# Optimization experiments

Measured on AMD Instinct MI355X. Metric: run time of the kernel, lower is better.

The kernel has to match this reference:

```python
import jax, jax.numpy as jnp
import numpy as np
from jax import lax

EPS = 1e-5

def conv2d(x, w, stride=1, pad=0):
    return lax.conv_general_dilated(x, w, (stride, stride), [(pad, pad), (pad, pad)],
                                    dimension_numbers=('NCHW', 'OIHW', 'NCHW'))

def bn_silu(x, p):
    # p: [4, C] = (gamma, beta, running_mean, running_var), eval-mode BN + SiLU
    g, b, m, v = p[0], p[1], p[2], p[3]
    scale = (g / jnp.sqrt(v + EPS))[None, :, None, None]
    y = (x - m[None, :, None, None]) * scale + b[None, :, None, None]
    return y * jax.nn.sigmoid(y)

def pixel_shuffle(x, r):
    N, C, H, W = x.shape
    C2 = C // (r * r)
    return x.reshape(N, C2, r, r, H, W).transpose(0, 1, 4, 2, 5, 3).reshape(N, C2, H * r, W * r)

def carafe_upsample(x, w_down, b_down, w_enc, b_enc, w_out, b_out, k=3, up=2):
    N, C, H, W = x.shape
    kt = conv2d(x, w_down) + b_down[None, :, None, None]            # [N, C//4, H, W]
    kt = conv2d(kt, w_enc, pad=k // 2) + b_enc[None, :, None, None]  # [N, up^2*k^2, H, W]
    kt = pixel_shuffle(kt, up)                                      # [N, k^2, H*up, W*up]
    kt = jax.nn.softmax(kt, axis=1)
    k2 = k * k
    # gather the up x up sub-blocks back per low-res position: [N, k2, H, W, up^2]
    kt = kt.reshape(N, k2, H, up, W, up).transpose(0, 1, 2, 4, 3, 5).reshape(N, k2, H, W, up * up)
    kt = kt.transpose(0, 2, 3, 1, 4)                                # [N, H, W, k2, up^2]
    # overlapping k x k input patches, zero-padded: [N, C*k2, H, W] with (C, kh, kw) channel order
    patches = lax.conv_general_dilated_patches(x, (k, k), (1, 1), [(k // 2, k // 2)] * 2)
    patches = patches.reshape(N, C, k2, H, W).transpose(0, 3, 4, 1, 2)  # [N, H, W, C, k2]
    out = jnp.einsum('nhwck,nhwkq->nhwcq', patches, kt)             # [N, H, W, C, up^2]
    out = out.reshape(N, H, W, C * up * up).transpose(0, 3, 1, 2)   # [N, C*up^2, H, W]
    out = pixel_shuffle(out, up)                                    # [N, C, H*up, W*up]
    return conv2d(out, w_out) + b_out[None, :, None, None]

def asff2_forward(input1, input2, w_down, b_down, w_enc, b_enc, w_up_out, b_up_out,
                  w_l1, bn_l1, w_l2, bn_l2, w_wl, b_wl, w_conv, bn_conv):
    # level == 0: upsample input2 to input1's resolution
    input2u = carafe_upsample(input2, w_down, b_down, w_enc, b_enc, w_up_out, b_up_out)
    v1 = bn_silu(conv2d(input1, w_l1), bn_l1)        # [N, 8, H, W]
    v2 = bn_silu(conv2d(input2u, w_l2), bn_l2)       # [N, 8, H, W]
    v = jnp.concatenate([v1, v2], axis=1)            # [N, 16, H, W]
    lw = conv2d(v, w_wl) + b_wl[None, :, None, None]  # [N, 2, H, W]
    lw = jax.nn.softmax(lw, axis=1)
    fused = input1 * lw[:, 0:1] + input2u * lw[:, 1:2]
    return bn_silu(conv2d(fused, w_conv, pad=1), bn_conv)


def _bn_params(key, c):
    ks = jax.random.split(key, 4)
    return jnp.stack([jax.random.uniform(ks[0], (c,)) + 0.5,
                      0.1 * jax.random.normal(ks[1], (c,)),
                      0.1 * jax.random.normal(ks[2], (c,)),
                      jax.random.uniform(ks[3], (c,)) + 0.5])


def setup_inputs() -> dict:
    key = jax.random.key(0)
    ks = jax.random.split(key, 20)
    N, C1, C2, H, W = 8, 256, 512, 64, 64
    s = 0.05  # small weight scale for numerical stability
    return {
        'input1': jax.random.normal(ks[0], (N, C1, H, W), jnp.float32),
        'input2': jax.random.normal(ks[1], (N, C2, H // 2, W // 2), jnp.float32),
        'w_down': s * jax.random.normal(ks[2], (C2 // 4, C2, 1, 1), jnp.float32),
        'b_down': s * jax.random.normal(ks[3], (C2 // 4,), jnp.float32),
        'w_enc': s * jax.random.normal(ks[4], (36, C2 // 4, 3, 3), jnp.float32),
        'b_enc': s * jax.random.normal(ks[5], (36,), jnp.float32),
        'w_up_out': s * jax.random.normal(ks[6], (C1, C2, 1, 1), jnp.float32),
        'b_up_out': s * jax.random.normal(ks[7], (C1,), jnp.float32),
        'w_l1': s * jax.random.normal(ks[8], (8, C1, 1, 1), jnp.float32),
        'bn_l1': _bn_params(ks[9], 8),
        'w_l2': s * jax.random.normal(ks[10], (8, C1, 1, 1), jnp.float32),
        'bn_l2': _bn_params(ks[11], 8),
        'w_wl': s * jax.random.normal(ks[12], (2, 16, 1, 1), jnp.float32),
        'b_wl': s * jax.random.normal(ks[13], (2,), jnp.float32),
        'w_conv': s * jax.random.normal(ks[14], (C1, C1, 3, 3), jnp.float32),
        'bn_conv': _bn_params(ks[15], C1),
    }


def reference(input1, input2, w_down, b_down, w_enc, b_enc, w_up_out, b_up_out,
              w_l1, bn_l1, w_l2, bn_l2, w_wl, b_wl, w_conv, bn_conv):
    return asff2_forward(input1, input2, w_down, b_down, w_enc, b_enc, w_up_out, b_up_out,
                         w_l1, bn_l1, w_l2, bn_l2, w_wl, b_wl, w_conv, bn_conv)
```

## Files before the change

### kernel.cpp

```cpp
#include <hip/hip_runtime.h>
#include <math.h>


#define EPS 1e-5f
typedef unsigned short u16;
typedef __attribute__((ext_vector_type(8))) __bf16 bf16x8;
typedef __attribute__((ext_vector_type(4))) float f32x4;

#define VMCNT(N) asm volatile("s_waitcnt vmcnt(" #N ")" ::: "memory")

__device__ inline u16 f2bf(float x) {
    union { float f; unsigned u; } v; v.f = x;
    unsigned r = v.u + 0x7FFF + ((v.u >> 16) & 1);
    return (u16)(r >> 16);
}
__device__ inline float bf2f(u16 x) {
    union { unsigned u; float f; } v; v.u = (unsigned)x << 16; return v.f;
}

#define STAGE_A(dstp, t, kx)                                                         \
    {                                                                                \
        const u16* Abase = A + ((long)(t) * 256 + rowBase) * KCC + (kx) * 32;        \
        _Pragma("unroll")                                                            \
        for (int ii = 0; ii < 2; ++ii) {                                             \
            int f = ii * 256 + tid;                                                  \
            int r = f >> 2, uu = f & 3;                                              \
            __builtin_amdgcn_global_load_lds(                                        \
                (const __attribute__((address_space(1))) void*)                      \
                    (Abase + (long)r * KCC + ((uu ^ ((r >> 1) & 3)) << 3)),          \
                (__attribute__((address_space(3))) void*)((dstp) + f * 8),           \
                16, 0, 0);                                                           \
        }                                                                            \
    }

#define STAGE_B(dstp, kx)                                                            \
    {                                                                                \
        const u16* Bbase = Bn + (long)g0 * KCC + (kx) * 32;                          \
        for (int f = tid; f < BUNITS; f += 256) {                                    \
            int r = f >> 2, uu = f & 3;                                              \
            __builtin_amdgcn_global_load_lds(                                        \
                (const __attribute__((address_space(1))) void*)                      \
                    (Bbase + (long)r * KCC + ((uu ^ ((r >> 1) & 3)) << 3)),          \
                (__attribute__((address_space(3))) void*)((dstp) + f * 8),           \
                16, 0, 0);                                                           \
        }                                                                            \
    }

__global__ __launch_bounds__(256, 2) void lowres_gemm_kernel(
    const u16* __restrict__ Aup,
    const u16* __restrict__ Adn,
    const u16* __restrict__ B,
    const float* __restrict__ bias,
    u16* __restrict__ Z,
    u16* __restrict__ ktT)
{
    constexpr int KCC = 512;
    constexpr int BUNITS = 512;
    __shared__ __align__(16) u16 lsA[3][128 * 32];
    __shared__ __align__(16) u16 lsB[3][128 * 32];
    const int n = blockIdx.z;
    const u16* Bn = B + (long)n * 1024 * 512;
    const int tid = threadIdx.x;
    const int lane = tid & 63;
    const int wid = tid >> 6;
    const int mw = wid >> 1, nw = wid & 1;
    const int lr = lane & 15, lk = lane >> 4;
    const int ybr = blockIdx.y;
    const u16* A = (ybr < 2) ? Aup : Adn;
    const int rowBase = (ybr < 2) ? ybr * 128 : 0;
    const int colBase = blockIdx.x * 128;
    const int g0 = colBase;

    STAGE_A(lsA[0], 0, 0); STAGE_B(lsB[0], 0);
    STAGE_A(lsA[1], 0, 1); STAGE_B(lsB[1], 1);

    const int aswz = (lk ^ ((lr >> 1) & 3)) << 3;
    int aoff[4];
#pragma unroll
    for (int mf = 0; mf < 4; ++mf)
        aoff[mf] = (mw * 64 + mf * 16 + lr) * 32 + aswz;

    f32x4 acc[4][4] = {};
    for (int kx = 0; kx < 16; ++kx) {
        if (kx == 15) { VMCNT(0); } else { VMCNT(4); }
        __builtin_amdgcn_s_barrier();
        asm volatile("" ::: "memory");
        if (kx + 2 < 16) {
            STAGE_A(lsA[(kx + 2) % 3], 0, kx + 2);
            STAGE_B(lsB[(kx + 2) % 3], kx + 2);
        }
        const u16* la = lsA[kx % 3];
        const u16* lb = lsB[kx % 3];
        bf16x8 af[4], bfr[4];
#pragma unroll
        for (int mf = 0; mf < 4; ++mf)
            af[mf] = *(const bf16x8*)(la + aoff[mf]);
        const int rb = nw * 64 + lr;
        const int bswz = (lk ^ ((rb >> 1) & 3)) << 3;
#pragma unroll
        for (int nf = 0; nf < 4; ++nf)
            bfr[nf] = *(const bf16x8*)(lb + (rb + nf * 16) * 32 + bswz);
#pragma unroll
        for (int mf = 0; mf < 4; ++mf)
#pragma unroll
            for (int nf = 0; nf < 4; ++nf)
                acc[mf][nf] = __builtin_amdgcn_mfma_f32_16x16x32_bf16(
                    af[mf], bfr[nf], acc[mf][nf], 0, 0, 0);
    }

    if (ybr < 2) {
        u16* Zn = Z + (long)n * 1024 * 256;
#pragma unroll
        for (int mf = 0; mf < 4; ++mf) {
            const int co0 = rowBase + mw * 64 + mf * 16 + lk * 4;
#pragma unroll
            for (int nf = 0; nf < 4; ++nf) {
                const int col = colBase + nw * 64 + nf * 16 + lr;
                unsigned lo = (unsigned)f2bf(acc[mf][nf][0]) |
                              ((unsigned)f2bf(acc[mf][nf][1]) << 16);
                unsigned hi = (unsigned)f2bf(acc[mf][nf][2]) |
                              ((unsigned)f2bf(acc[mf][nf][3]) << 16);
                *(uint2*)(Zn + (long)col * 256 + co0) = make_uint2(lo, hi);
            }
        }
    } else {
        u16* Kn = ktT + (long)n * 1156 * 128;
#pragma unroll
        for (int mf = 0; mf < 4; ++mf) {
            const int co0 = mw * 64 + mf * 16 + lk * 4;
            float b0 = bias[co0], b1 = bias[co0 + 1], b2 = bias[co0 + 2], b3 = bias[co0 + 3];
#pragma unroll
            for (int nf = 0; nf < 4; ++nf) {
                const int col = colBase + nw * 64 + nf * 16 + lr;
                const int pr = ((col >> 5) + 1) * 34 + (col & 31) + 1;
                unsigned lo = (unsigned)f2bf(acc[mf][nf][0] + b0) |
                              ((unsigned)f2bf(acc[mf][nf][1] + b1) << 16);
                unsigned hi = (unsigned)f2bf(acc[mf][nf][2] + b2) |
                              ((unsigned)f2bf(acc[mf][nf][3] + b3) << 16);
                *(uint2*)(Kn + (long)pr * 128 + co0) = make_uint2(lo, hi);
            }
        }
    }
}

__global__ __launch_bounds__(64) void encsm_zw_kernel(
    const u16* __restrict__ A, const u16* __restrict__ B,
    const float* __restrict__ bias,
    const u16* __restrict__ zbfT, const float* __restrict__ wl2T,
    float* __restrict__ mask, float* __restrict__ zwT)
{
    const int bid = blockIdx.x;
    const int lane = threadIdx.x;
    if (bid < 512) {
        const int n = bid >> 6;
        const int lr = lane & 15, lk = lane >> 4;
        const int p = (bid & 63) * 16 + lr;
        const int pr = ((p >> 5) + 1) * 34 + (p & 31) + 1;
        const u16* Bn = B + (long)n * 1156 * 128;
        const int bOff = pr * 128 + lk * 8;
        f32x4 acc[3] = {};
        for (int t = 0; t < 9; ++t) {
            const u16* At = A + t * 8192;
            const int btap = ((t / 3 - 1) * 34 + (t % 3 - 1)) * 128;
#pragma unroll
            for (int k0 = 0; k0 < 128; k0 += 32) {
                bf16x8 bf = *(const bf16x8*)(Bn + bOff + btap + k0);
#pragma unroll
                for (int mf = 0; mf < 3; ++mf) {
                    bf16x8 af = *(const bf16x8*)(At + (mf * 16 + lr) * 128 + lk * 8 + k0);
                    acc[mf] = __builtin_amdgcn_mfma_f32_16x16x32_bf16(af, bf, acc[mf], 0, 0, 0);
                }
            }
        }
        float* mp = mask + ((long)n * 1024 + p) * 36;
#pragma unroll
        for (int q = 0; q < 4; ++q) {
            float v0 = acc[0][q] + bias[lk * 4 + q];
            float v1 = acc[1][q] + bias[16 + lk * 4 + q];
            float v2 = (lk == 0) ? (acc[2][q] + bias[32 + q]) : -1e30f;
            float m = fmaxf(fmaxf(v0, v1), v2);
            m = fmaxf(m, __shfl_xor(m, 16, 64));
            m = fmaxf(m, __shfl_xor(m, 32, 64));
            float e0 = expf(v0 - m);
            float e1 = expf(v1 - m);
            float e2 = (lk == 0) ? expf(v2 - m) : 0.f;
            float s = e0 + e1 + e2;
            s += __shfl_xor(s, 16, 64);
            s += __shfl_xor(s, 32, 64);
            float inv = 1.f / s;
            mp[lk * 4 + q] = e0 * inv;
            mp[16 + lk * 4 + q] = e1 * inv;
            if (lk == 0) mp[32 + q] = e2 * inv;
        }
    } else {
        const int Q = bid - 512;
        const int ci0 = lane * 4;
        uint2 v = *(const uint2*)(zbfT + (long)Q * 256 + ci0);
        float c[4] = { bf2f((u16)(v.x & 0xffff)), bf2f((u16)(v.x >> 16)),
                       bf2f((u16)(v.y & 0xffff)), bf2f((u16)(v.y >> 16)) };
        float s[8] = {};
#pragma unroll
        for (int t = 0; t < 4; ++t) {
            const float* wr = wl2T + (ci0 + t) * 8;
            float4 wa = *(const float4*)wr;
            float4 wb = *(const float4*)(wr + 4);
            s[0] += wa.x * c[t]; s[1] += wa.y * c[t]; s[2] += wa.z * c[t]; s[3] += wa.w * c[t];
            s[4] += wb.x * c[t]; s[5] += wb.y * c[t]; s[6] += wb.z * c[t]; s[7] += wb.w * c[t];
        }
#pragma unroll
        for (int off = 1; off < 64; off <<= 1)
#pragma unroll
            for (int j = 0; j < 8; ++j)
                s[j] += __shfl_xor(s[j], off, 64);
        if (lane == 0) {
            float* o = zwT + (long)Q * 8;
            *(float4*)o = make_float4(s[0], s[1], s[2], s[3]);
            *(float4*)(o + 4) = make_float4(s[4], s[5], s[6], s[7]);
        }
    }
}

__global__ __launch_bounds__(256) void carafe_fuse_blend_kernel(
    const float* __restrict__ i1g, const u16* __restrict__ zbfT,
    const float* __restrict__ zwT, const float* __restrict__ maskb,
    const float* __restrict__ bnp,
    const float* __restrict__ w_l1, const float* __restrict__ bn_l1,
    const float* __restrict__ bn_l2, const float* __restrict__ w_wl,
    const float* __restrict__ b_wl, u16* __restrict__ dst)
{
    __shared__ float lw0s[32];
    __shared__ __align__(16) unsigned char uscr[32 * 264 * 2];
    float* red = (float*)uscr;
    u16* lds2 = (u16*)uscr;
    const int n = blockIdx.y;
    const int h = blockIdx.x >> 1;
    const int w0 = (blockIdx.x & 1) << 5;
    const int hq = h >> 1;
    const int tid = threadIdx.x;

    const int w = tid & 31;
    const int chunk = tid >> 5;
    const float* i1 = i1g + (long)n * 256 * 4096 + (h << 6) + w0 + w;
    float i1v[32];
    {
        float s1[8] = {};
#pragma unroll
        for (int i = 0; i < 32; ++i) {
            const int ci = chunk * 32 + i;
            float x1 = i1[(long)ci * 4096];
            i1v[i] = x1;
#pragma unroll
            for (int j = 0; j < 8; ++j) s1[j] += w_l1[j * 256 + ci] * x1;
        }
#pragma unroll
        for (int j = 0; j < 8; ++j) red[(chunk * 32 + w) * 8 + j] = s1[j];
    }
    __syncthreads();
    {
        int px = tid >> 3, j = tid & 7;
        float s = 0.f;
#pragma unroll
        for (int o = 0; o < 8; ++o) s += red[(o * 32 + px) * 8 + j];
        red[px * 8 + j] = s;
    }
    __syncthreads();
    if (tid < 32) {
        const int wp = w0 + tid;
        const int wq = wp >> 1;
        const int q = ((h & 1) << 1) | (wp & 1);
        const float* mrow = maskb + ((long)n * 1024 + hq * 32 + wq) * 36;
        float v[16];
#pragma unroll
        for (int j = 0; j < 8; ++j) v[j] = red[tid * 8 + j];
#pragma unroll
        for (int j = 0; j < 8; ++j) v[8 + j] = bnp[512 + j];
#pragma unroll
        for (int k = 0; k < 9; ++k) {
            int dh = k / 3 - 1, dw = k - (k / 3) * 3 - 1;
            int gr = hq + dh, gc = wq + dw;
            bool ok = (gr >= 0 && gr < 32 && gc >= 0 && gc < 32);
            float mk = ok ? mrow[k * 4 + q] : 0.f;
            const float* zp = zwT + ((long)n * 1024 +
                                     (ok ? gr * 32 + gc : hq * 32 + wq)) * 8;
            float4 za = *(const float4*)zp;
            float4 zb = *(const float4*)(zp + 4);
            v[8]  += mk * za.x; v[9]  += mk * za.y; v[10] += mk * za.z; v[11] += mk * za.w;
            v[12] += mk * zb.x; v[13] += mk * zb.y; v[14] += mk * zb.z; v[15] += mk * zb.w;
        }
        float z0 = b_wl[0], z1 = b_wl[1];
#pragma unroll
        for (int j = 0; j < 8; ++j) {
            float g = bn_l1[j], b = bn_l1[8 + j], m = bn_l1[16 + j], va = bn_l1[24 + j];
            float y = (v[j] - m) * (g * rsqrtf(va + EPS)) + b;
            float sv = y / (1.f + expf(-y));
            z0 += w_wl[j] * sv;
            z1 += w_wl[16 + j] * sv;
            g = bn_l2[j]; b = bn_l2[8 + j]; m = bn_l2[16 + j]; va = bn_l2[24 + j];
            y = (v[8 + j] - m) * (g * rsqrtf(va + EPS)) + b;
            sv = y / (1.f + expf(-y));
            z0 += w_wl[8 + j] * sv;
            z1 += w_wl[24 + j] * sv;
        }
        lw0s[tid] = 1.f / (1.f + expf(z1 - z0));
    }
    __syncthreads();
    {
        const float lw = lw0s[w], lw1 = 1.f - lw;
        const int wp = w0 + w;
        const int wq = wp >> 1;
        const int q = ((h & 1) << 1) | (wp & 1);
        const float* mrow = maskb + ((long)n * 1024 + hq * 32 + wq) * 36;
        float m9[9];
        const u16* zp[9];
#pragma unroll
        for (int k = 0; k < 9; ++k) {
            int dh = k / 3 - 1, dw = k - (k / 3) * 3 - 1;
            int gr = hq + dh, gc = wq + dw;
            bool ok = (gr >= 0 && gr < 32 && gc >= 0 && gc < 32);
            m9[k] = ok ? mrow[k * 4 + q] : 0.f;
            zp[k] = zbfT + ((long)n * 1024 +
                            (ok ? gr * 32 + gc : hq * 32 + wq)) * 256;
        }
#pragma unroll
        for (int ci8 = 0; ci8 < 32; ci8 += 8) {
            const int ci = chunk * 32 + ci8;
            float uu[8];
            {
                float4 ba = *(const float4*)(bnp + 768 + ci);
                float4 bb = *(const float4*)(bnp + 768 + ci + 4);
                uu[0] = ba.x; uu[1] = ba.y; uu[2] = ba.z; uu[3] = ba.w;
                uu[4] = bb.x; uu[5] = bb.y; uu[6] = bb.z; uu[7] = bb.w;
            }
#pragma unroll
            for (int k = 0; k < 9; ++k) {
                uint4 vz = *(const uint4*)(zp[k] + ci);
                float mk = m9[k];
                uu[0] += mk * bf2f((u16)(vz.x & 0xffff));
                uu[1] += mk * bf2f((u16)(vz.x >> 16));
                uu[2] += mk * bf2f((u16)(vz.y & 0xffff));
                uu[3] += mk * bf2f((u16)(vz.y >> 16));
                uu[4] += mk * bf2f((u16)(vz.z & 0xffff));
                uu[5] += mk * bf2f((u16)(vz.z >> 16));
                uu[6] += mk * bf2f((u16)(vz.w & 0xffff));
                uu[7] += mk * bf2f((u16)(vz.w >> 16));
            }
            unsigned o0 = (unsigned)f2bf(i1v[ci8 + 0] * lw + uu[0] * lw1)
                        | ((unsigned)f2bf(i1v[ci8 + 1] * lw + uu[1] * lw1) << 16);
            unsigned o1 = (unsigned)f2bf(i1v[ci8 + 2] * lw + uu[2] * lw1)
                        | ((unsigned)f2bf(i1v[ci8 + 3] * lw + uu[3] * lw1) << 16);
            unsigned o2 = (unsigned)f2bf(i1v[ci8 + 4] * lw + uu[4] * lw1)
                        | ((unsigned)f2bf(i1v[ci8 + 5] * lw + uu[5] * lw1) << 16);
            unsigned o3 = (unsigned)f2bf(i1v[ci8 + 6] * lw + uu[6] * lw1)
                        | ((unsigned)f2bf(i1v[ci8 + 7] * lw + uu[7] * lw1) << 16);
            *(uint4*)(lds2 + w * 264 + ci) = make_uint4(o0, o1, o2, o3);
        }
    }
    __syncthreads();
    {
        const int px = tid >> 3, qd = tid & 7;
        const int pg = (h << 6) + w0 + px;
        long prow = (long)((pg >> 6) + 1) * 66 + (pg & 63) + 1;
        u16* drow = dst + (long)n * 4356 * 256 + prow * 256;
        const u16* lrow = lds2 + px * 264;
#pragma unroll
        for (int j = 0; j < 16; ++j) {
            int off = j * 16 + qd * 2;
            *(unsigned*)(drow + off) = *(const unsigned*)(lrow + off);
        }
    }
}

template<int KCC, int NT, bool PADDED>
__global__ __launch_bounds__(256, 2) void gemm_m97_kernel(
    const u16* __restrict__ A,
    const u16* __restrict__ B,
    const float* __restrict__ scale, const float* __restrict__ shift,
    float* __restrict__ C, long strideB, long strideC, int silu)
{
    constexpr int RROWS = PADDED ? 264 : 128;
    constexpr int BUNITS = RROWS * 4;
    constexpr int NKX = KCC / 32;
    constexpr int MINB = BUNITS / 256;
    __shared__ __align__(16) u16 lsA[3][128 * 32];
    __shared__ __align__(16) u16 lsB[3][RROWS * 32];
    const int n = blockIdx.z;
    const u16* Bn = B + (long)n * strideB;
    float* Cn = C + (long)n * strideC;
    const int tid = threadIdx.x;
    const int lane = tid & 63;
    const int wid = tid >> 6;
    const int mw = wid >> 1, nw = wid & 1;
    const int lr = lane & 15, lk = lane >> 4;
    const int rowBase = blockIdx.y * 128;
    const int colBase = blockIdx.x * 128;
    const int g0 = PADDED ? (colBase >> 6) * 66 : colBase;

    STAGE_B(lsB[0], 0);
    STAGE_A(lsA[0], 0, 0);

    const int aswz = (lk ^ ((lr >> 1) & 3)) << 3;
    int aoff[4];
#pragma unroll
    for (int mf = 0; mf < 4; ++mf)
        aoff[mf] = (mw * 64 + mf * 16 + lr) * 32 + aswz;

    f32x4 acc[4][4] = {};
    for (int kx = 0; kx < NKX; ++kx) {
        const u16* lb = lsB[kx % 3];
#pragma unroll
        for (int t = 0; t < NT; ++t) {
            const int s = kx * NT + t;
            const bool lastS = (kx == NKX - 1) && (t == NT - 1);
            const bool stgB = (t == 0) && (kx + 1 < NKX);
            if (stgB) STAGE_B(lsB[(kx + 1) % 3], kx + 1);
            if (!lastS) {
                const int t1 = (t + 1 == NT) ? 0 : t + 1;
                const int kx1 = (t + 1 == NT) ? kx + 1 : kx;
                STAGE_A(lsA[(s + 1) % 3], t1, kx1);
            }
            if (lastS) { VMCNT(0); }
            else if (stgB) { if constexpr (MINB == 2) VMCNT(4); else VMCNT(6); }
            else { VMCNT(2); }
            __builtin_amdgcn_s_barrier();
            asm volatile("" ::: "memory");

            const u16* la = lsA[s % 3];
            bf16x8 af[4], bfr[4];
#pragma unroll
            for (int mf = 0; mf < 4; ++mf)
                af[mf] = *(const bf16x8*)(la + aoff[mf]);
            int rb;
            if (PADDED) {
                int dh = t / 3 - 1, dw = t - (t / 3) * 3 - 1;
                rb = (nw + dh + 1) * 66 + dw + 1 + lr;
            } else {
                rb = nw * 64 + lr;
            }
            const int bswz = (lk ^ ((rb >> 1) & 3)) << 3;
#pragma unroll
            for (int nf = 0; nf < 4; ++nf)
                bfr[nf] = *(const bf16x8*)(lb + (rb + nf * 16) * 32 + bswz);
#pragma unroll
            for (int mf = 0; mf < 4; ++mf)
#pragma unroll
                for (int nf = 0; nf < 4; ++nf)
                    acc[mf][nf] = __builtin_amdgcn_mfma_f32_16x16x32_bf16(
                        af[mf], bfr[nf], acc[mf][nf], 0, 0, 0);
        }
    }

#pragma unroll
    for (int mf = 0; mf < 4; ++mf) {
#pragma unroll
        for (int reg = 0; reg < 4; ++reg) {
            int co = rowBase + mw * 64 + mf * 16 + lk * 4 + reg;
            float sc = scale[co], sh = shift[co];
#pragma unroll
            for (int nf = 0; nf < 4; ++nf) {
                int col = colBase + nw * 64 + nf * 16 + lr;
                float y = acc[mf][nf][reg] * sc + sh;
                if (silu) y = y / (1.f + expf(-y));
                Cn[(long)co * 4096 + col] = y;
            }
        }
    }
}

__global__ __launch_bounds__(256) void prep_in2t_kernel(
    const float* __restrict__ input2, u16* __restrict__ in2T,
    const float* __restrict__ w_conv, const float* __restrict__ w_up,
    const float* __restrict__ w_enc, const float* __restrict__ w_down,
    const float* __restrict__ bn_conv, const float* __restrict__ b_up,
    const float* __restrict__ w_l2,
    u16* __restrict__ wT, u16* __restrict__ wupT, u16* __restrict__ wencT,
    u16* __restrict__ wdT, u16* __restrict__ ftb, u16* __restrict__ ktT,
    float* __restrict__ bnp, float* __restrict__ wl2T)
{
    constexpr int CP = 264;
    __shared__ u16 lds[64 * CP];
    const int bid = blockIdx.x;
    const int tid = threadIdx.x;
    if (bid < 256) {
        const int n = bid >> 5;
        const int c0 = ((bid >> 4) & 1) << 8;
        const int p0 = (bid & 15) * 64;
        {
            const int px = tid & 63;
            const float* src = input2 + (long)n * 512 * 1024 + (long)c0 * 1024 + p0 + px;
            for (int ci = tid >> 6; ci < 256; ci += 4)
                lds[px * CP + ci] = f2bf(src[(long)ci * 1024]);
        }
        __syncthreads();
        const int px = tid >> 2;
        const int qd = tid & 3;
        u16* drow = in2T + ((long)n * 1024 + p0 + px) * 512 + c0;
        const u16* lrow = lds + px * CP;
#pragma unroll
        for (int j = 0; j < 8; ++j) {
            int off = j * 32 + qd * 8;
            *(uint4*)(drow + off) = *(const uint4*)(lrow + off);
        }
        return;
    }
    if (bid < 2560) {
        int gid = (bid - 256) * 256 + tid;
        if (gid < 589824) {
            int t = gid >> 16;
            int co = (gid >> 8) & 255;
            int ci = gid & 255;
            wT[gid] = f2bf(w_conv[(co * 256 + ci) * 9 + t]);
        }
        if (gid < 131072) wupT[gid] = f2bf(w_up[gid]);
        if (gid < 73728) {
            int t = gid >> 13;
            int co = (gid >> 7) & 63;
            int ci = gid & 127;
            wencT[gid] = (co < 36) ? f2bf(w_enc[(co * 128 + ci) * 9 + t]) : (u16)0;
        }
        if (gid < 65536) wdT[gid] = f2bf(w_down[gid]);
        return;
    }
    if (bid < 2886) {
        int gid = (bid - 2560) * 256 + tid;
        if (gid < 8 * 260 * 32) {
            int n = gid / (260 * 32);
            int rem = gid - n * (260 * 32);
            int r = rem >> 5;
            int i = rem & 31;
            int h, w;
            if (r < 66)       { h = 0;  w = r; }
            else if (r < 132) { h = 65; w = r - 66; }
            else { int j = r - 132; h = 1 + (j >> 1); w = (j & 1) * 65; }
            long prow = (long)h * 66 + w;
            uint4* dst = (uint4*)(ftb + (long)n * 4356 * 256 + prow * 256) + i;
            *dst = make_uint4(0, 0, 0, 0);
            return;
        }
        int g2 = gid - 8 * 260 * 32;
        if (g2 >= 8 * 132 * 16) return;
        int n = g2 / (132 * 16);
        int rem = g2 - n * (132 * 16);
        int r = rem >> 4;
        int i = rem & 15;
        int h, w;
        if (r < 34)      { h = 0;  w = r; }
        else if (r < 68) { h = 33; w = r - 34; }
        else { int j = r - 68; h = 1 + (j >> 1); w = (j & 1) * 33; }
        long prow = (long)h * 34 + w;
        uint4* dst = (uint4*)(ktT + (long)n * 1156 * 128 + prow * 128) + i;
        *dst = make_uint4(0, 0, 0, 0);
        return;
    }
    {
        int i = tid;
        float g = bn_conv[i], b = bn_conv[256 + i], m = bn_conv[512 + i], v = bn_conv[768 + i];
        float sc = g * rsqrtf(v + EPS);
        bnp[i] = sc;
        bnp[256 + i] = b - m * sc;
        bnp[768 + i] = b_up[i];
        if (i < 8) {
            float s = 0.f;
            for (int co = 0; co < 256; ++co) s += w_l2[i * 256 + co] * b_up[co];
            bnp[512 + i] = s;
        }
#pragma unroll
        for (int j = 0; j < 8; ++j)
            wl2T[i * 8 + j] = w_l2[j * 256 + i];
    }
}

extern "C" void kernel_launch(void* const* d_in, const int* in_sizes, int n_in,
                              void* d_out, int out_size, void* d_ws, size_t ws_size,
                              hipStream_t stream)
{
    const float* input1 = (const float*)d_in[0];
    const float* input2 = (const float*)d_in[1];
    const float* w_down = (const float*)d_in[2];
    const float* b_down = (const float*)d_in[3];
    const float* w_enc  = (const float*)d_in[4];
    const float* b_enc  = (const float*)d_in[5];
    const float* w_up   = (const float*)d_in[6];
    const float* b_up   = (const float*)d_in[7];
    const float* w_l1   = (const float*)d_in[8];
    const float* bn_l1  = (const float*)d_in[9];
    const float* w_l2   = (const float*)d_in[10];
    const float* bn_l2  = (const float*)d_in[11];
    const float* w_wl   = (const float*)d_in[12];
    const float* b_wl   = (const float*)d_in[13];
    const float* w_conv = (const float*)d_in[14];
    const float* bn_conv= (const float*)d_in[15];
    float* out = (float*)d_out;

    float* ws     = (float*)d_ws;
    float* ktTf   = ws;
    float* wencTf = ktTf + 591872;
    float* maskb  = wencTf + 36864;
    float* in2Tf  = maskb + 294912;
    float* zbfTf  = in2Tf + 2097152;
    float* zwT    = zbfTf + 1048576;
    float* ftbf   = zwT + 65536;
    float* wTf    = ftbf + 4460544;
    float* wupTf  = wTf + 294912;
    float* wdTf   = wupTf + 65536;
    float* wl2T   = wdTf + 32768;
    float* bnp    = wl2T + 2048;
    u16* ktT      = (u16*)ktTf;
    u16* wencT    = (u16*)wencTf;
    u16* in2T     = (u16*)in2Tf;
    u16* zbfT     = (u16*)zbfTf;
    u16* ftb      = (u16*)ftbf;
    u16* wT       = (u16*)wTf;
    u16* wupT     = (u16*)wupTf;
    u16* wdT      = (u16*)wdTf;

    prep_in2t_kernel<<<dim3(2887), 256, 0, stream>>>(
        input2, in2T, w_conv, w_up, w_enc, w_down, bn_conv, b_up, w_l2,
        wT, wupT, wencT, wdT, ftb, ktT, bnp, wl2T);

    lowres_gemm_kernel<<<dim3(8, 3, 8), 256, 0, stream>>>(
        wupT, wdT, in2T, b_down, zbfT, ktT);

    encsm_zw_kernel<<<dim3(512 + 8192), 64, 0, stream>>>(
        wencT, ktT, b_enc, zbfT, wl2T, maskb, zwT);

    carafe_fuse_blend_kernel<<<dim3(128, 8), 256, 0, stream>>>(
        input1, zbfT, zwT, maskb, bnp, w_l1, bn_l1, bn_l2, w_wl, b_wl, ftb);

    gemm_m97_kernel<256, 9, true><<<dim3(32, 2, 8), 256, 0, stream>>>(
        wT, ftb, bnp, bnp + 256, out, 4356L * 256, 256L * 4096, 1);
}
```

Baseline: 122.9 us.

## Move input1 level-weight projection into the low-res GEMM launch as extra blocks

The 1x1 projection of input1 to 8 channels (w_l1) is moved out of the blend kernel into extra blocks appended to the low-res GEMM grid. Those blocks write per-pixel sums to a new workspace buffer, which the blend kernel then reads. The GEMM uses only 192 blocks, so the projection is meant to fill idle CUs and to shorten the blend kernel's critical path, including one barrier and its LDS reduction. In exchange, input1 is read twice from global memory (once for the projection, once for the blend, which no longer keeps it in registers), and there is an extra small buffer round trip.

```diff
diff --git a/kernel.cpp b/kernel.cpp
--- a/kernel.cpp
+++ b/kernel.cpp
@@ -51,24 +51,57 @@
     const u16* __restrict__ Adn,
     const u16* __restrict__ B,
     const float* __restrict__ bias,
+    const float* __restrict__ i1g, const float* __restrict__ w_l1,
     u16* __restrict__ Z,
-    u16* __restrict__ ktT)
+    u16* __restrict__ ktT,
+    float* __restrict__ v1buf)
 {
     constexpr int KCC = 512;
     constexpr int BUNITS = 512;
     __shared__ __align__(16) u16 lsA[3][128 * 32];
     __shared__ __align__(16) u16 lsB[3][128 * 32];
-    const int n = blockIdx.z;
+    const int bid0 = blockIdx.x;
+    const int tid = threadIdx.x;
+
+    if (bid0 >= 192) {
+        float* red = (float*)lsA;
+        const int vb = bid0 - 192;
+        const int n = vb >> 7;
+        const int hw = vb & 127;
+        const int h = hw >> 1;
+        const int w0 = (hw & 1) << 5;
+        const int w = tid & 31;
+        const int chunk = tid >> 5;
+        const float* i1 = i1g + (long)n * 256 * 4096 + (h << 6) + w0 + w;
+        float s1[8] = {};
+        for (int i = 0; i < 32; ++i) {
+            const int ci = chunk * 32 + i;
+            float x1 = i1[(long)ci * 4096];
+#pragma unroll
+            for (int j = 0; j < 8; ++j) s1[j] += w_l1[j * 256 + ci] * x1;
+        }
+#pragma unroll
+        for (int j = 0; j < 8; ++j) red[(chunk * 32 + w) * 8 + j] = s1[j];
+        __syncthreads();
+        const int px = tid >> 3, j = tid & 7;
+        float s = 0.f;
+#pragma unroll
+        for (int o = 0; o < 8; ++o) s += red[(o * 32 + px) * 8 + j];
+        v1buf[((long)n * 4096 + (h << 6) + w0 + px) * 8 + j] = s;
+        return;
+    }
+
+    const int xb = bid0 & 7;
+    const int ybr = (bid0 >> 3) % 3;
+    const int n = bid0 / 24;
     const u16* Bn = B + (long)n * 1024 * 512;
-    const int tid = threadIdx.x;
     const int lane = tid & 63;
     const int wid = tid >> 6;
     const int mw = wid >> 1, nw = wid & 1;
     const int lr = lane & 15, lk = lane >> 4;
-    const int ybr = blockIdx.y;
     const u16* A = (ybr < 2) ? Aup : Adn;
     const int rowBase = (ybr < 2) ? ybr * 128 : 0;
-    const int colBase = blockIdx.x * 128;
+    const int colBase = xb * 128;
     const int g0 = colBase;
 
     STAGE_A(lsA[0], 0, 0); STAGE_B(lsB[0], 0);
@@ -224,54 +257,33 @@
     const float* __restrict__ i1g, const u16* __restrict__ zbfT,
     const float* __restrict__ zwT, const float* __restrict__ maskb,
     const float* __restrict__ bnp,
-    const float* __restrict__ w_l1, const float* __restrict__ bn_l1,
+    const float* __restrict__ v1buf, const float* __restrict__ bn_l1,
     const float* __restrict__ bn_l2, const float* __restrict__ w_wl,
     const float* __restrict__ b_wl, u16* __restrict__ dst)
 {
     __shared__ float lw0s[32];
-    __shared__ __align__(16) unsigned char uscr[32 * 264 * 2];
-    float* red = (float*)uscr;
-    u16* lds2 = (u16*)uscr;
+    __shared__ __align__(16) u16 lds2[32 * 264];
     const int n = blockIdx.y;
     const int h = blockIdx.x >> 1;
     const int w0 = (blockIdx.x & 1) << 5;
     const int hq = h >> 1;
     const int tid = threadIdx.x;
-
     const int w = tid & 31;
     const int chunk = tid >> 5;
-    const float* i1 = i1g + (long)n * 256 * 4096 + (h << 6) + w0 + w;
-    float i1v[32];
-    {
-        float s1[8] = {};
-#pragma unroll
-        for (int i = 0; i < 32; ++i) {
-            const int ci = chunk * 32 + i;
-            float x1 = i1[(long)ci * 4096];
-            i1v[i] = x1;
-#pragma unroll
-            for (int j = 0; j < 8; ++j) s1[j] += w_l1[j * 256 + ci] * x1;
-        }
-#pragma unroll
-        for (int j = 0; j < 8; ++j) red[(chunk * 32 + w) * 8 + j] = s1[j];
-    }
-    __syncthreads();
-    {
-        int px = tid >> 3, j = tid & 7;
-        float s = 0.f;
-#pragma unroll
-        for (int o = 0; o < 8; ++o) s += red[(o * 32 + px) * 8 + j];
-        red[px * 8 + j] = s;
-    }
-    __syncthreads();
+
     if (tid < 32) {
         const int wp = w0 + tid;
         const int wq = wp >> 1;
         const int q = ((h & 1) << 1) | (wp & 1);
         const float* mrow = maskb + ((long)n * 1024 + hq * 32 + wq) * 36;
         float v[16];
-#pragma unroll
-        for (int j = 0; j < 8; ++j) v[j] = red[tid * 8 + j];
+        {
+            const float* vp = v1buf + ((long)n * 4096 + (h << 6) + wp) * 8;
+            float4 va = *(const float4*)vp;
+            float4 vb = *(const float4*)(vp + 4);
+            v[0] = va.x; v[1] = va.y; v[2] = va.z; v[3] = va.w;
+            v[4] = vb.x; v[5] = vb.y; v[6] = vb.z; v[7] = vb.w;
+        }
 #pragma unroll
         for (int j = 0; j < 8; ++j) v[8 + j] = bnp[512 + j];
 #pragma unroll
@@ -309,6 +321,7 @@
         const int wp = w0 + w;
         const int wq = wp >> 1;
         const int q = ((h & 1) << 1) | (wp & 1);
+        const float* i1 = i1g + (long)n * 256 * 4096 + (h << 6) + w0 + w;
         const float* mrow = maskb + ((long)n * 1024 + hq * 32 + wq) * 36;
         float m9[9];
         const u16* zp[9];
@@ -321,9 +334,7 @@
             zp[k] = zbfT + ((long)n * 1024 +
                             (ok ? gr * 32 + gc : hq * 32 + wq)) * 256;
         }
-#pragma unroll
-        for (int ci8 = 0; ci8 < 32; ci8 += 8) {
-            const int ci = chunk * 32 + ci8;
+        for (int ci = chunk * 32; ci < chunk * 32 + 32; ci += 8) {
             float uu[8];
             {
                 float4 ba = *(const float4*)(bnp + 768 + ci);
@@ -344,14 +355,14 @@
                 uu[6] += mk * bf2f((u16)(vz.w & 0xffff));
                 uu[7] += mk * bf2f((u16)(vz.w >> 16));
             }
-            unsigned o0 = (unsigned)f2bf(i1v[ci8 + 0] * lw + uu[0] * lw1)
-                        | ((unsigned)f2bf(i1v[ci8 + 1] * lw + uu[1] * lw1) << 16);
-            unsigned o1 = (unsigned)f2bf(i1v[ci8 + 2] * lw + uu[2] * lw1)
-                        | ((unsigned)f2bf(i1v[ci8 + 3] * lw + uu[3] * lw1) << 16);
-            unsigned o2 = (unsigned)f2bf(i1v[ci8 + 4] * lw + uu[4] * lw1)
-                        | ((unsigned)f2bf(i1v[ci8 + 5] * lw + uu[5] * lw1) << 16);
-            unsigned o3 = (unsigned)f2bf(i1v[ci8 + 6] * lw + uu[6] * lw1)
-                        | ((unsigned)f2bf(i1v[ci8 + 7] * lw + uu[7] * lw1) << 16);
+            unsigned o0 = (unsigned)f2bf(i1[(long)ci * 4096] * lw + uu[0] * lw1)
+                        | ((unsigned)f2bf(i1[(long)(ci + 1) * 4096] * lw + uu[1] * lw1) << 16);
+            unsigned o1 = (unsigned)f2bf(i1[(long)(ci + 2) * 4096] * lw + uu[2] * lw1)
+                        | ((unsigned)f2bf(i1[(long)(ci + 3) * 4096] * lw + uu[3] * lw1) << 16);
+            unsigned o2 = (unsigned)f2bf(i1[(long)(ci + 4) * 4096] * lw + uu[4] * lw1)
+                        | ((unsigned)f2bf(i1[(long)(ci + 5) * 4096] * lw + uu[5] * lw1) << 16);
+            unsigned o3 = (unsigned)f2bf(i1[(long)(ci + 6) * 4096] * lw + uu[6] * lw1)
+                        | ((unsigned)f2bf(i1[(long)(ci + 7) * 4096] * lw + uu[7] * lw1) << 16);
             *(uint4*)(lds2 + w * 264 + ci) = make_uint4(o0, o1, o2, o3);
         }
     }
@@ -604,6 +615,7 @@
     float* wdTf   = wupTf + 65536;
     float* wl2T   = wdTf + 32768;
     float* bnp    = wl2T + 2048;
+    float* v1buf  = bnp + 1024;
     u16* ktT      = (u16*)ktTf;
     u16* wencT    = (u16*)wencTf;
     u16* in2T     = (u16*)in2Tf;
@@ -617,14 +629,14 @@
         input2, in2T, w_conv, w_up, w_enc, w_down, bn_conv, b_up, w_l2,
         wT, wupT, wencT, wdT, ftb, ktT, bnp, wl2T);
 
-    lowres_gemm_kernel<<<dim3(8, 3, 8), 256, 0, stream>>>(
-        wupT, wdT, in2T, b_down, zbfT, ktT);
+    lowres_gemm_kernel<<<dim3(192 + 1024), 256, 0, stream>>>(
+        wupT, wdT, in2T, b_down, input1, w_l1, zbfT, ktT, v1buf);
 
     encsm_zw_kernel<<<dim3(512 + 8192), 64, 0, stream>>>(
         wencT, ktT, b_enc, zbfT, wl2T, maskb, zwT);
 
     carafe_fuse_blend_kernel<<<dim3(128, 8), 256, 0, stream>>>(
-        input1, zbfT, zwT, maskb, bnp, w_l1, bn_l1, bn_l2, w_wl, b_wl, ftb);
+        input1, zbfT, zwT, maskb, bnp, v1buf, bn_l1, bn_l2, w_wl, b_wl, ftb);
 
     gemm_m97_kernel<256, 9, true><<<dim3(32, 2, 8), 256, 0, stream>>>(
         wT, ftb, bnp, bnp + 256, out, 4356L * 256, 256L * 4096, 1);
```

Measured after the change: 118.2 us, median of 2. 3.8% less time.
